# Kernel optimization log

Hardware: AMD Instinct MI355X
Metric: run time of the kernel (lower is better)

Reference implementation:

```python
import jax, jax.numpy as jnp
import numpy as np

B, S, DIM, H = 2, 2048, 1024, 16
DH = DIM // H            # 64
G = DH // 4              # 16 quaternion groups per head
IQ = DIM // 4            # 256
ROPE_BASE = 10000.0
SCALE = DH ** -0.5


def qlinear(x, wr, wi, wj, wk, b):
    # x: [B,S,4*IQ]; strided quaternion components, exact combo from QuaternionLinear.forward
    xr, xi, xj, xk = x[..., 0::4], x[..., 1::4], x[..., 2::4], x[..., 3::4]
    o_r = xr @ wr.T - xi @ wi.T - xj @ wj.T - xk @ wk.T
    o_i = xi @ wr.T + xr @ wi.T + xk @ wk.T - xj @ wj.T
    o_j = xj @ wr.T - xk @ wk.T + xr @ wj.T + xi @ wi.T
    o_k = xk @ wr.T + xj @ wj.T - xi @ wi.T + xr @ wk.T
    out = jnp.stack([o_r, o_i, o_j, o_k], axis=-1).reshape(x.shape[:-1] + (-1,))
    return out + b


def qrope(x):
    # x: [B,H,S,DH]; left quaternion multiply u(theta) \otimes q, axis_mode='cycle'
    b, h, s, dh = x.shape
    g = dh // 4
    xq = x.reshape(b, h, s, g, 4)
    t = jnp.arange(s, dtype=x.dtype)
    inv = 1.0 / (ROPE_BASE ** (jnp.arange(g, dtype=x.dtype) / g))
    ang = t[:, None] * inv[None, :]            # [S,G]
    cos, sin = jnp.cos(ang), jnp.sin(ang)
    gi = jnp.arange(g)
    ax_i = (gi % 3 == 0).astype(x.dtype)
    ax_j = (gi % 3 == 1).astype(x.dtype)
    ax_k = (gi % 3 == 2).astype(x.dtype)
    ur, ui, uj, uk = cos, sin * ax_i, sin * ax_j, sin * ax_k   # [S,G] broadcast over [B,H,S,G]
    xr, xi, xj, xk = xq[..., 0], xq[..., 1], xq[..., 2], xq[..., 3]
    pr = ur * xr - ui * xi - uj * xj - uk * xk
    pi = ur * xi + ui * xr + uj * xk - uk * xj
    pj = ur * xj - ui * xk + uj * xr + uk * xi
    pk = ur * xk + ui * xj - uj * xi + uk * xr
    return jnp.stack([pr, pi, pj, pk], axis=-1).reshape(b, h, s, dh)


def setup_inputs() -> dict:
    key = jax.random.key(0)
    ks = jax.random.split(key, 24)
    x = jax.random.normal(ks[0], (B, S, DIM), dtype=jnp.float32)
    # causal mask: True = masked
    mask = jnp.broadcast_to(jnp.triu(jnp.ones((S, S), dtype=bool), k=1), (B, S, S))
    inp = {"x": x, "mask": mask}
    i = 1
    for proj in ("q", "k", "v", "o"):
        for comp in ("wr", "wi", "wj", "wk"):
            inp[f"{proj}_{comp}"] = jax.random.normal(ks[i], (IQ, IQ), dtype=jnp.float32) * 0.02
            i += 1
        inp[f"{proj}_b"] = jnp.zeros((DIM,), dtype=jnp.float32)
    return inp


def reference(x, mask,
              q_wr, q_wi, q_wj, q_wk, q_b,
              k_wr, k_wi, k_wj, k_wk, k_b,
              v_wr, v_wi, v_wj, v_wk, v_b,
              o_wr, o_wi, o_wj, o_wk, o_b):
    b, s, dm = x.shape
    q = qlinear(x, q_wr, q_wi, q_wj, q_wk, q_b).reshape(b, s, H, DH).transpose(0, 2, 1, 3)
    k = qlinear(x, k_wr, k_wi, k_wj, k_wk, k_b).reshape(b, s, H, DH).transpose(0, 2, 1, 3)
    v = qlinear(x, v_wr, v_wi, v_wj, v_wk, v_b).reshape(b, s, H, DH).transpose(0, 2, 1, 3)
    q, k = qrope(q), qrope(k)
    scores = jnp.einsum('bhsd,bhtd->bhst', q, k) * SCALE
    scores = jnp.where(mask[:, None, :, :], -jnp.inf, scores)
    a = jax.nn.softmax(scores, axis=-1)
    out = jnp.einsum('bhst,bhtd->bhsd', a, v).transpose(0, 2, 1, 3).reshape(b, s, dm)
    return qlinear(out, o_wr, o_wi, o_wj, o_wk, o_b)
```

## Files before the change

kernel.cpp:

```cpp
#include <hip/hip_runtime.h>
#include <stdint.h>

typedef unsigned short u16;
typedef unsigned int   u32;

#define NB   2
#define NS   2048
#define NDIM 1024
#define NH   16
#define NDH  64
#define QSCALE 0.18033688011112042f

typedef __bf16 bf16x8 __attribute__((ext_vector_type(8)));
typedef float  f32x4  __attribute__((ext_vector_type(4)));

#define MFMA_BF16(a,b,c) __builtin_amdgcn_mfma_f32_16x16x32_bf16((a),(b),(c),0,0,0)

#define XBF_OFF   (256)
#define WD_OFF    (XBF_OFF  + 8*1024*1024)
#define BIAS_OFF  (WD_OFF   + 8*1024*1024)
#define QB_OFF    (BIAS_OFF + 16384)
#define KB_OFF    (QB_OFF   + 8*1024*1024)
#define VT_OFF    (KB_OFF   + 8*1024*1024)
#define OP_OFF    (VT_OFF   + 8*1024*1024)
#define LP_OFF    (OP_OFF   + 16*1024*1024)

__device__ __forceinline__ float bf2f(u16 h){
  union { u32 u; float f; } v; v.u = ((u32)h) << 16; return v.f;
}
__device__ __forceinline__ u16 f2bf(float f){
  union { float f; u32 u; } v; v.f = f;
  u32 r = (v.u >> 16) & 1u;
  return (u16)((v.u + 0x7fffu + r) >> 16);
}
__device__ __forceinline__ float load_val(const void* p, int i, int isbf){
  return isbf ? bf2f(((const u16*)p)[i]) : ((const float*)p)[i];
}
__device__ __forceinline__ void gl_lds16(const u16* g, u16* l){
  __builtin_amdgcn_global_load_lds(
      (__attribute__((address_space(1))) void*)(uintptr_t)g,
      (__attribute__((address_space(3))) void*)(uintptr_t)l,
      16, 0, 0);
}

struct QPtrs { const void* w[16]; const void* b[4]; };

__global__ void prep_kernel(const void* __restrict__ xin, QPtrs ptrs,
                            u16* __restrict__ xbf, u16* __restrict__ wd,
                            float* __restrict__ biasf, int* __restrict__ flag){
  __shared__ int cnt;
  if (threadIdx.x == 0) cnt = 0;
  __syncthreads();
  {
    const uint4* xv = (const uint4*)xin;
    uint4 v0 = xv[threadIdx.x * 2], v1 = xv[threadIdx.x * 2 + 1];
    const u16* hh = (const u16*)&v0;
    int ok = 0;
#pragma unroll
    for (int i = 0; i < 16; ++i){
      u16 h = (i < 8) ? hh[i] : ((const u16*)&v1)[i - 8];
      int e = (h >> 7) & 0xFF;
      if ((e > 96 && e < 158) || ((h & 0x7FFF) == 0)) ok++;
    }
    atomicAdd(&cnt, ok);
  }
  __syncthreads();
  int isbf = (cnt > 3600) ? 1 : 0;
  if (blockIdx.x == 0 && threadIdx.x == 0) *flag = isbf;

  int idx = blockIdx.x * 256 + threadIdx.x;

  if (blockIdx.x < 2048){
    int t = idx;
    if (isbf){
      ((uint4*)xbf)[t] = ((const uint4*)xin)[t];
    } else {
      const float4* f4 = (const float4*)xin;
      float4 a = f4[2*t], b = f4[2*t+1];
      ushort4 lo = { f2bf(a.x), f2bf(a.y), f2bf(a.z), f2bf(a.w) };
      ushort4 hi = { f2bf(b.x), f2bf(b.y), f2bf(b.z), f2bf(b.w) };
      ((ushort4*)xbf)[2*t]   = lo;
      ((ushort4*)xbf)[2*t+1] = hi;
    }
  }

  int n = idx & 255, m = (idx >> 8) & 255, c = (idx >> 16) & 3, p = idx >> 18;
  int src = m * 256 + n;
  float vr = load_val(ptrs.w[p*4+0], src, isbf);
  float vi = load_val(ptrs.w[p*4+1], src, isbf);
  float vj = load_val(ptrs.w[p*4+2], src, isbf);
  float vk = load_val(ptrs.w[p*4+3], src, isbf);
  float o0, o1, o2, o3;
  switch (c){
    case 0:  o0 = vr; o1 = -vi; o2 = -vj; o3 = -vk; break;
    case 1:  o0 = vi; o1 =  vr; o2 = -vj; o3 =  vk; break;
    case 2:  o0 = vj; o1 =  vi; o2 =  vr; o3 = -vk; break;
    default: o0 = vk; o1 = -vi; o2 =  vj; o3 =  vr; break;
  }
  ushort4 sv = { f2bf(o0), f2bf(o1), f2bf(o2), f2bf(o3) };
  *(ushort4*)&wd[(size_t)p * 1048576 + (size_t)(4*m + c) * 1024 + 4*n] = sv;
  if (idx < 4096){
    int pp = idx >> 10, oo = idx & 1023;
    biasf[idx] = load_val(ptrs.b[pp], oo, isbf);
  }
}

__global__ __launch_bounds__(256)
void gemm_qkv_kernel(const u16* __restrict__ A, const u16* __restrict__ Bw,
                     const float* __restrict__ bias,
                     u16* __restrict__ qb, u16* __restrict__ kb, u16* __restrict__ vt){
  __shared__ u16 sA[3][128 * 32];
  __shared__ u16 sB[3][128 * 32];
  int tid = threadIdx.x, w = tid >> 6, lane = tid & 63, quad = lane >> 4, l16 = lane & 15;
  int n0 = blockIdx.x * 128, m0 = blockIdx.y * 128;

  f32x4 acc[4][4];
#pragma unroll
  for (int i = 0; i < 4; ++i)
#pragma unroll
    for (int j = 0; j < 4; ++j) acc[i][j] = (f32x4){0.f, 0.f, 0.f, 0.f};

  int cp = lane & 3, rl = lane >> 2;
  int gc = (cp ^ ((rl >> 1) & 3)) * 8;
  const u16* ga = A  + (size_t)(m0 + w*16 + rl) * 1024 + gc;
  const u16* gb = Bw + (size_t)(n0 + w*16 + rl) * 1024 + gc;
  int ldo = w * 512 + lane * 8;
  int xorv = ((l16 >> 1) & 3) * 8;
  int mw = (w & 1) * 64, nw = (w >> 1) * 64;

  auto stage = [&](int k0, int b){
#pragma unroll
    for (int i = 0; i < 2; ++i){
      gl_lds16(ga + (size_t)i * 65536 + k0, &sA[b][ldo + i * 2048]);
      gl_lds16(gb + (size_t)i * 65536 + k0, &sB[b][ldo + i * 2048]);
    }
  };

  stage(0, 0);
  stage(32, 1);
  asm volatile("s_waitcnt vmcnt(4)" ::: "memory");
  __builtin_amdgcn_s_barrier();

  int bcur = 0, bnxt = 2;
  for (int it = 0; it < 32; ++it){
    if (it < 30) stage((it + 2) * 32, bnxt);
    const u16* cA = sA[bcur];
    const u16* cB = sB[bcur];
    bf16x8 af[4], bfr[4];
#pragma unroll
    for (int mt = 0; mt < 4; ++mt)
      af[mt] = *(const bf16x8*)&cA[(mw + mt*16 + l16) * 32 + (quad*8 ^ xorv)];
#pragma unroll
    for (int nt = 0; nt < 4; ++nt)
      bfr[nt] = *(const bf16x8*)&cB[(nw + nt*16 + l16) * 32 + (quad*8 ^ xorv)];
#pragma unroll
    for (int mt = 0; mt < 4; ++mt)
#pragma unroll
      for (int nt = 0; nt < 4; ++nt)
        acc[mt][nt] = MFMA_BF16(af[mt], bfr[nt], acc[mt][nt]);

    if (it < 30) asm volatile("s_waitcnt vmcnt(4)" ::: "memory");
    else         asm volatile("s_waitcnt vmcnt(0)" ::: "memory");
    __builtin_amdgcn_s_barrier();
    bcur = (bcur == 2) ? 0 : bcur + 1;
    bnxt = (bnxt == 2) ? 0 : bnxt + 1;
  }

  int proj = n0 >> 10;
  if (proj == 2){
#pragma unroll
    for (int mt = 0; mt < 4; ++mt){
      int row = m0 + mw + mt*16 + quad*4;
      int b = row >> 11, seq0 = row & 2047;
#pragma unroll
      for (int nt = 0; nt < 4; ++nt){
        int col = n0 + nw + nt*16 + l16;
        int o = col & 1023, h = o >> 6, d = o & 63;
        float bv = bias[col];
        ushort4 pv = { f2bf(acc[mt][nt][0] + bv), f2bf(acc[mt][nt][1] + bv),
                       f2bf(acc[mt][nt][2] + bv), f2bf(acc[mt][nt][3] + bv) };
        *(ushort4*)&vt[((size_t)((b*16 + h) * 64 + d)) * 2048 + seq0] = pv;
      }
    }
  } else {
    float sc = (proj == 0) ? QSCALE : 1.0f;
    u16* dst = proj ? kb : qb;
    int c = l16 & 3;
#pragma unroll
    for (int nt = 0; nt < 4; ++nt){
      int col = n0 + nw + nt*16 + l16;
      int o = col & 1023, h = o >> 6, d = o & 63;
      int g = d >> 2;
      int ax = g % 3;
      int mask = ax + 1;
      int tbl = (ax == 0) ? 0xA : (ax == 1 ? 0x6 : 0xC);
      float sgn = ((tbl >> c) & 1) ? 1.f : -1.f;
      float inv = __builtin_amdgcn_exp2f(-(float)g * 0.8304820237218405f);
      float bv = bias[col];
#pragma unroll
      for (int mt = 0; mt < 4; ++mt){
        int row0 = m0 + mw + mt*16 + quad*4;
        int b = row0 >> 11, s0 = row0 & 2047;
        size_t obase = ((size_t)((b*16 + h) * 2048 + s0)) * 64 + d;
#pragma unroll
        for (int r = 0; r < 4; ++r){
          float v = acc[mt][nt][r] + bv;
          float vp = __shfl_xor(v, mask);
          float ang = (float)(s0 + r) * inv;
          float co = __cosf(ang) * sc;
          float si = __sinf(ang) * sc * sgn;
          dst[obase + (size_t)r * 64] = f2bf(co * v + si * vp);
        }
      }
    }
  }
}

__global__ __launch_bounds__(256)
void gemm_o_kernel(const u16* __restrict__ A, const u16* __restrict__ Bw,
                   const float* __restrict__ bias, void* __restrict__ dout,
                   const int* __restrict__ flag){
  __shared__ u16 sA[3][64 * 32];
  __shared__ u16 sB[3][128 * 32];
  int tid = threadIdx.x, w = tid >> 6, lane = tid & 63, quad = lane >> 4, l16 = lane & 15;
  int n0 = blockIdx.x * 128, m0 = blockIdx.y * 64;

  f32x4 acc[2][4];
#pragma unroll
  for (int i = 0; i < 2; ++i)
#pragma unroll
    for (int j = 0; j < 4; ++j) acc[i][j] = (f32x4){0.f, 0.f, 0.f, 0.f};

  int cp = lane & 3, rl = lane >> 2;
  int gc = (cp ^ ((rl >> 1) & 3)) * 8;
  int xorv = ((l16 >> 1) & 3) * 8;
  int mw = (w & 1) * 32, nw = (w >> 1) * 64;

  auto stage = [&](int k0, int b){
#pragma unroll
    for (int i = 0; i < 3; ++i){
      int ch = w * 3 + i;
      int lr = (ch < 4 ? ch : ch - 4) * 16 + rl;
      int eo = (ch < 4 ? ch : ch - 4) * 512 + lane * 8;
      if (ch < 4) gl_lds16(A  + (size_t)(m0 + lr) * 1024 + k0 + gc, &sA[b][eo]);
      else        gl_lds16(Bw + (size_t)(n0 + lr) * 1024 + k0 + gc, &sB[b][eo]);
    }
  };

  stage(0, 0);
  stage(32, 1);
  asm volatile("s_waitcnt vmcnt(3)" ::: "memory");
  __builtin_amdgcn_s_barrier();

  int bcur = 0, bnxt = 2;
  for (int it = 0; it < 32; ++it){
    if (it < 30) stage((it + 2) * 32, bnxt);
    const u16* cA = sA[bcur];
    const u16* cB = sB[bcur];
    bf16x8 af[2], bfr[4];
#pragma unroll
    for (int mt = 0; mt < 2; ++mt)
      af[mt] = *(const bf16x8*)&cA[(mw + mt*16 + l16) * 32 + (quad*8 ^ xorv)];
#pragma unroll
    for (int nt = 0; nt < 4; ++nt)
      bfr[nt] = *(const bf16x8*)&cB[(nw + nt*16 + l16) * 32 + (quad*8 ^ xorv)];
#pragma unroll
    for (int mt = 0; mt < 2; ++mt)
#pragma unroll
      for (int nt = 0; nt < 4; ++nt)
        acc[mt][nt] = MFMA_BF16(af[mt], bfr[nt], acc[mt][nt]);

    if (it < 30) asm volatile("s_waitcnt vmcnt(3)" ::: "memory");
    else         asm volatile("s_waitcnt vmcnt(0)" ::: "memory");
    __builtin_amdgcn_s_barrier();
    bcur = (bcur == 2) ? 0 : bcur + 1;
    bnxt = (bnxt == 2) ? 0 : bnxt + 1;
  }

  int isbf = *flag;
#pragma unroll
  for (int mt = 0; mt < 2; ++mt){
    int row = m0 + mw + mt*16 + quad*4;
#pragma unroll
    for (int nt = 0; nt < 4; ++nt){
      int col = n0 + nw + nt*16 + l16;
      float bv = bias[col];
#pragma unroll
      for (int r = 0; r < 4; ++r){
        float val = acc[mt][nt][r] + bv;
        size_t addr = (size_t)(row + r) * 1024 + col;
        if (isbf) ((u16*)dout)[addr] = f2bf(val);
        else      ((float*)dout)[addr] = val;
      }
    }
  }
}

#define SPT 20

__global__ __launch_bounds__(256, 2)
void attn_kernel(const u16* __restrict__ Q, const u16* __restrict__ K,
                 const u16* __restrict__ Vt, u16* __restrict__ OP,
                 float* __restrict__ LP){
  __shared__ u16 sK[2][4096];
  __shared__ u16 sPT[4][64 * SPT];
  int bh  = blockIdx.x;
  int spl = blockIdx.y;
  int tid = threadIdx.x, w = tid >> 6, lane = tid & 63, quad = lane >> 4, l16 = lane & 15;
  size_t kbase = (size_t)bh * 2048 * 64;
  size_t vbase = (size_t)bh * 64 * 2048;
  u16* spw = &sPT[w][0];

  auto stage = [&](int kt, int b){
    int kcol = kt * 64;
#pragma unroll
    for (int p = 0; p < 2; ++p){
      int slot = w*128 + p*64 + lane;
      int row = slot >> 3, dc = (slot & 7) ^ (row & 7);
      gl_lds16(K + kbase + (size_t)(kcol + row) * 64 + dc*8, &sK[b][(w*128 + p*64) * 8]);
    }
  };

  for (int item = 0; item < 2; ++item){
    int qt = item ? (int)blockIdx.z : 15 - (int)blockIdx.z;
    int rowbase = qt * 128 + w * 32;

    bf16x8 qf[2][2];
#pragma unroll
    for (int g = 0; g < 2; ++g)
#pragma unroll
      for (int kc = 0; kc < 2; ++kc)
        qf[g][kc] = *(const bf16x8*)(Q + kbase + (size_t)(rowbase + g*16 + l16) * 64 + kc*32 + quad*8);

    f32x4 oaccT[2][4];
    float lsum[2][4];
#pragma unroll
    for (int g = 0; g < 2; ++g)
#pragma unroll
      for (int i = 0; i < 4; ++i){ oaccT[g][i] = (f32x4){0.f,0.f,0.f,0.f}; lsum[g][i] = 0.f; }

    int kt0 = spl ? (qt + 1) : 0;
    int ntiles = qt + 1;

    stage(kt0, 0);
    for (int i = 0; i < ntiles; ++i){
      int kcol = (kt0 + i) * 64;
      __syncthreads();
      if (i + 1 < ntiles) stage(kt0 + i + 1, (i + 1) & 1);
      const u16* bK = sK[i & 1];

      if (kcol <= rowbase + 31){
        bf16x8 vf[4][2];
#pragma unroll
        for (int dn = 0; dn < 4; ++dn)
#pragma unroll
          for (int kc = 0; kc < 2; ++kc)
            vf[dn][kc] = *(const bf16x8*)(Vt + vbase + (size_t)(dn*16 + l16) * 2048
                                          + kcol + kc*32 + quad*8);
        bf16x8 bk[2][4];
#pragma unroll
        for (int kc = 0; kc < 2; ++kc)
#pragma unroll
          for (int nt = 0; nt < 4; ++nt){
            int rw = nt*16 + l16;
            int ch = ((kc*4 + quad) ^ (rw & 7)) * 8;
            bk[kc][nt] = *(const bf16x8*)&bK[rw*64 + ch];
          }
#pragma unroll
        for (int g = 0; g < 2; ++g){
          int G0 = rowbase + g*16;
          if (kcol <= G0 + 15){
            f32x4 sacc[4];
#pragma unroll
            for (int nt = 0; nt < 4; ++nt) sacc[nt] = (f32x4){0.f,0.f,0.f,0.f};
#pragma unroll
            for (int kc = 0; kc < 2; ++kc)
#pragma unroll
              for (int nt = 0; nt < 4; ++nt)
                sacc[nt] = MFMA_BF16(qf[g][kc], bk[kc][nt], sacc[nt]);

            if (kcol + 63 > G0){
#pragma unroll
              for (int nt = 0; nt < 4; ++nt){
                int col = kcol + nt*16 + l16;
                ushort4 pv;
#pragma unroll
                for (int r = 0; r < 4; ++r){
                  int row = G0 + quad*4 + r;
                  float pp = (col <= row) ? __builtin_amdgcn_exp2f(sacc[nt][r]) : 0.f;
                  lsum[g][r] += pp;
                  ((u16*)&pv)[r] = f2bf(pp);
                }
                *(ushort4*)&spw[(nt*16 + l16) * SPT + quad*4] = pv;
              }
            } else {
#pragma unroll
              for (int nt = 0; nt < 4; ++nt){
                ushort4 pv;
#pragma unroll
                for (int r = 0; r < 4; ++r){
                  float pp = __builtin_amdgcn_exp2f(sacc[nt][r]);
                  lsum[g][r] += pp;
                  ((u16*)&pv)[r] = f2bf(pp);
                }
                *(ushort4*)&spw[(nt*16 + l16) * SPT + quad*4] = pv;
              }
            }
#pragma unroll
            for (int kc = 0; kc < 2; ++kc){
              bf16x8 pf;
#pragma unroll
              for (int j = 0; j < 8; ++j)
                pf[j] = ((const __bf16*)spw)[(kc*32 + quad*8 + j) * SPT + l16];
#pragma unroll
              for (int dn = 0; dn < 4; ++dn)
                oaccT[g][dn] = MFMA_BF16(vf[dn][kc], pf, oaccT[g][dn]);
            }
          }
        }
      }
    }

    float* scr = (float*)spw;
#pragma unroll
    for (int g = 0; g < 2; ++g)
#pragma unroll
      for (int r = 0; r < 4; ++r){
        float l = lsum[g][r];
        l += __shfl_xor(l, 1); l += __shfl_xor(l, 2);
        l += __shfl_xor(l, 4); l += __shfl_xor(l, 8);
        if (l16 == 0) scr[g*16 + quad*4 + r] = l;
      }
    float lrow[2];
#pragma unroll
    for (int g = 0; g < 2; ++g) lrow[g] = scr[g*16 + l16];

    size_t obase = ((size_t)(spl*32 + bh)) * 2048;
#pragma unroll
    for (int g = 0; g < 2; ++g){
      int row = rowbase + g*16 + l16;
      if (quad == 0) LP[obase + row] = lrow[g];
#pragma unroll
      for (int dn = 0; dn < 4; ++dn){
        ushort4 ov = { f2bf(oaccT[g][dn][0]), f2bf(oaccT[g][dn][1]),
                       f2bf(oaccT[g][dn][2]), f2bf(oaccT[g][dn][3]) };
        *(ushort4*)&OP[(obase + row) * 64 + dn*16 + quad*4] = ov;
      }
    }

    __syncthreads();
  }
}

__global__ void combine_kernel(const u16* __restrict__ OP, const float* __restrict__ LP,
                               u16* __restrict__ Ab){
  int idx = blockIdx.x * 256 + threadIdx.x;
  int dc = idx & 7, s = (idx >> 3) & 2047, bh = idx >> 14;
  size_t r0 = (size_t)bh * 2048 + s, r1 = (size_t)(32 + bh) * 2048 + s;
  float invl = 1.f / (LP[r0] + LP[r1]);
  union { uint4 v; u16 h[8]; } a0, a1; ushort4 o[2];
  a0.v = *(const uint4*)&OP[r0 * 64 + dc*8];
  a1.v = *(const uint4*)&OP[r1 * 64 + dc*8];
#pragma unroll
  for (int p = 0; p < 2; ++p)
#pragma unroll
    for (int j = 0; j < 4; ++j)
      ((u16*)&o[p])[j] = f2bf((bf2f(a0.h[p*4+j]) + bf2f(a1.h[p*4+j])) * invl);
  int b = bh >> 4, h = bh & 15;
  u16* dst = &Ab[((size_t)(b*2048 + s)) * 1024 + h*64 + dc*8];
  *(ushort4*)dst = o[0];
  *(ushort4*)(dst + 4) = o[1];
}

extern "C" void kernel_launch(void* const* d_in, const int* in_sizes, int n_in,
                              void* d_out, int out_size, void* d_ws, size_t ws_size,
                              hipStream_t stream){
  (void)in_sizes; (void)n_in; (void)out_size; (void)ws_size;
  char* ws = (char*)d_ws;
  int*   flag  = (int*)ws;
  u16*   Xbf   = (u16*)(ws + XBF_OFF);
  u16*   Wd    = (u16*)(ws + WD_OFF);
  float* biasf = (float*)(ws + BIAS_OFF);
  u16*   Qb    = (u16*)(ws + QB_OFF);
  u16*   Kb    = (u16*)(ws + KB_OFF);
  u16*   Vt    = (u16*)(ws + VT_OFF);
  u16*   OP    = (u16*)(ws + OP_OFF);
  float* LP    = (float*)(ws + LP_OFF);
  u16*   Ab    = Xbf;

  QPtrs ptrs;
  for (int p = 0; p < 4; ++p){
    for (int wi = 0; wi < 4; ++wi) ptrs.w[p*4 + wi] = d_in[2 + p*5 + wi];
    ptrs.b[p] = d_in[2 + p*5 + 4];
  }

  prep_kernel<<<4096, 256, 0, stream>>>(d_in[0], ptrs, Xbf, Wd, biasf, flag);
  gemm_qkv_kernel<<<dim3(24, 32), 256, 0, stream>>>(Xbf, Wd, biasf, Qb, Kb, Vt);
  attn_kernel<<<dim3(32, 2, 8), 256, 0, stream>>>(Qb, Kb, Vt, OP, LP);
  combine_kernel<<<2048, 256, 0, stream>>>(OP, LP, Ab);
  gemm_o_kernel<<<dim3(8, 64), 256, 0, stream>>>(Ab, Wd + 3*1048576, biasf + 3072,
                                                 d_out, flag);
}
```

Baseline: 244.4 us.

## Enlarge QKV GEMM tile to 256x256 with 512 threads and split-phase staging

The QKV projection GEMM now uses a 256x256 output tile per block with 8 waves, each wave computing a 128x64 sub-tile in two halves. Staging of A and B tiles is split across the two compute halves, with explicit LDS waits, scheduling barriers and wave priority raised around the MFMA bursts. The aim is more operand reuse per LDS load and better overlap of global-to-LDS copies with matrix math. In exchange the grid shrinks to 192 blocks, which may underfill the GPU, and register and LDS pressure per block rise.

New measurement: 241.6 us. About the same (-1.1%).

```diff
diff --git a/kernel.cpp b/kernel.cpp
--- a/kernel.cpp
+++ b/kernel.cpp
@@ -105,76 +105,113 @@
   }
 }
 
-__global__ __launch_bounds__(256)
+__global__ __launch_bounds__(512, 2)
 void gemm_qkv_kernel(const u16* __restrict__ A, const u16* __restrict__ Bw,
                      const float* __restrict__ bias,
                      u16* __restrict__ qb, u16* __restrict__ kb, u16* __restrict__ vt){
-  __shared__ u16 sA[3][128 * 32];
-  __shared__ u16 sB[3][128 * 32];
-  int tid = threadIdx.x, w = tid >> 6, lane = tid & 63, quad = lane >> 4, l16 = lane & 15;
-  int n0 = blockIdx.x * 128, m0 = blockIdx.y * 128;
-
-  f32x4 acc[4][4];
-#pragma unroll
-  for (int i = 0; i < 4; ++i)
+  __shared__ u16 sA[3][256 * 32];
+  __shared__ u16 sB[3][256 * 32];
+  int tid = threadIdx.x, lane = tid & 63, quad = lane >> 4, l16 = lane & 15;
+  int wid = tid >> 6;
+  int wr = wid >> 2, wc = wid & 3;
+  int mbase = wr * 128, nbase = wc * 64;
+  int n0 = blockIdx.x * 256, m0 = blockIdx.y * 256;
+
+  f32x4 acc[8][4];
+#pragma unroll
+  for (int i = 0; i < 8; ++i)
 #pragma unroll
     for (int j = 0; j < 4; ++j) acc[i][j] = (f32x4){0.f, 0.f, 0.f, 0.f};
 
-  int cp = lane & 3, rl = lane >> 2;
-  int gc = (cp ^ ((rl >> 1) & 3)) * 8;
-  const u16* ga = A  + (size_t)(m0 + w*16 + rl) * 1024 + gc;
-  const u16* gb = Bw + (size_t)(n0 + w*16 + rl) * 1024 + gc;
-  int ldo = w * 512 + lane * 8;
-  int xorv = ((l16 >> 1) & 3) * 8;
-  int mw = (w & 1) * 64, nw = (w >> 1) * 64;
-
-  auto stage = [&](int k0, int b){
-#pragma unroll
-    for (int i = 0; i < 2; ++i){
-      gl_lds16(ga + (size_t)i * 65536 + k0, &sA[b][ldo + i * 2048]);
-      gl_lds16(gb + (size_t)i * 65536 + k0, &sB[b][ldo + i * 2048]);
-    }
+  const u16* gA = A  + (size_t)m0 * 1024;
+  const u16* gB = Bw + (size_t)n0 * 1024;
+  int r0s = tid >> 2,            c0s = tid & 3;
+  int r1s = (tid + 512) >> 2,    c1s = (tid + 512) & 3;
+  int sa0 = r0s * 1024 + (c0s ^ ((r0s >> 1) & 3)) * 8;
+  int sa1 = r1s * 1024 + (c1s ^ ((r1s >> 1) & 3)) * 8;
+  int d0 = tid * 8, d1 = (tid + 512) * 8;
+
+  auto stage_A = [&](int t, int b){
+    int k0 = t * 32;
+    gl_lds16(gA + sa0 + k0, &sA[b][d0]);
+    gl_lds16(gA + sa1 + k0, &sA[b][d1]);
   };
-
-  stage(0, 0);
-  stage(32, 1);
+  auto stage_B = [&](int t, int b){
+    int k0 = t * 32;
+    gl_lds16(gB + sa0 + k0, &sB[b][d0]);
+    gl_lds16(gB + sa1 + k0, &sB[b][d1]);
+  };
+
+  int xo = (quad ^ ((l16 >> 1) & 3)) * 8;
+
+  stage_A(0, 0); stage_B(0, 0);
+  stage_A(1, 1); stage_B(1, 1);
   asm volatile("s_waitcnt vmcnt(4)" ::: "memory");
   __builtin_amdgcn_s_barrier();
 
-  int bcur = 0, bnxt = 2;
-  for (int it = 0; it < 32; ++it){
-    if (it < 30) stage((it + 2) * 32, bnxt);
+  int bcur = 0, bst = 2;
+  for (int t = 0; t < 32; ++t){
     const u16* cA = sA[bcur];
     const u16* cB = sB[bcur];
-    bf16x8 af[4], bfr[4];
-#pragma unroll
-    for (int mt = 0; mt < 4; ++mt)
-      af[mt] = *(const bf16x8*)&cA[(mw + mt*16 + l16) * 32 + (quad*8 ^ xorv)];
-#pragma unroll
-    for (int nt = 0; nt < 4; ++nt)
-      bfr[nt] = *(const bf16x8*)&cB[(nw + nt*16 + l16) * 32 + (quad*8 ^ xorv)];
-#pragma unroll
-    for (int mt = 0; mt < 4; ++mt)
+
+    if (t < 30) stage_A(t + 2, bst);
+    {
+      bf16x8 af[4], bfr[4];
+#pragma unroll
+      for (int mt = 0; mt < 4; ++mt)
+        af[mt] = *(const bf16x8*)&cA[(mbase + mt*16 + l16) * 32 + xo];
 #pragma unroll
       for (int nt = 0; nt < 4; ++nt)
-        acc[mt][nt] = MFMA_BF16(af[mt], bfr[nt], acc[mt][nt]);
-
-    if (it < 30) asm volatile("s_waitcnt vmcnt(4)" ::: "memory");
-    else         asm volatile("s_waitcnt vmcnt(0)" ::: "memory");
+        bfr[nt] = *(const bf16x8*)&cB[(nbase + nt*16 + l16) * 32 + xo];
+      asm volatile("s_waitcnt lgkmcnt(0)" ::: "memory");
+      __builtin_amdgcn_sched_barrier(0);
+      __builtin_amdgcn_s_setprio(1);
+#pragma unroll
+      for (int mt = 0; mt < 4; ++mt)
+#pragma unroll
+        for (int nt = 0; nt < 4; ++nt)
+          acc[mt][nt] = MFMA_BF16(af[mt], bfr[nt], acc[mt][nt]);
+      __builtin_amdgcn_s_setprio(0);
+    }
     __builtin_amdgcn_s_barrier();
+
+    if (t < 30) stage_B(t + 2, bst);
+    {
+      bf16x8 af[4], bfr[4];
+#pragma unroll
+      for (int mt = 0; mt < 4; ++mt)
+        af[mt] = *(const bf16x8*)&cA[(mbase + (4+mt)*16 + l16) * 32 + xo];
+#pragma unroll
+      for (int nt = 0; nt < 4; ++nt)
+        bfr[nt] = *(const bf16x8*)&cB[(nbase + nt*16 + l16) * 32 + xo];
+      asm volatile("s_waitcnt lgkmcnt(0)" ::: "memory");
+      __builtin_amdgcn_sched_barrier(0);
+      __builtin_amdgcn_s_setprio(1);
+#pragma unroll
+      for (int mt = 0; mt < 4; ++mt)
+#pragma unroll
+        for (int nt = 0; nt < 4; ++nt)
+          acc[4+mt][nt] = MFMA_BF16(af[mt], bfr[nt], acc[4+mt][nt]);
+      __builtin_amdgcn_s_setprio(0);
+    }
+    if (t < 31){
+      if (t < 30) asm volatile("s_waitcnt vmcnt(4)" ::: "memory");
+      else        asm volatile("s_waitcnt vmcnt(0)" ::: "memory");
+      __builtin_amdgcn_s_barrier();
+    }
     bcur = (bcur == 2) ? 0 : bcur + 1;
-    bnxt = (bnxt == 2) ? 0 : bnxt + 1;
+    bst  = (bst  == 2) ? 0 : bst  + 1;
   }
 
   int proj = n0 >> 10;
   if (proj == 2){
 #pragma unroll
-    for (int mt = 0; mt < 4; ++mt){
-      int row = m0 + mw + mt*16 + quad*4;
+    for (int mt = 0; mt < 8; ++mt){
+      int row = m0 + mbase + mt*16 + quad*4;
       int b = row >> 11, seq0 = row & 2047;
 #pragma unroll
       for (int nt = 0; nt < 4; ++nt){
-        int col = n0 + nw + nt*16 + l16;
+        int col = n0 + nbase + nt*16 + l16;
         int o = col & 1023, h = o >> 6, d = o & 63;
         float bv = bias[col];
         ushort4 pv = { f2bf(acc[mt][nt][0] + bv), f2bf(acc[mt][nt][1] + bv),
@@ -188,7 +225,7 @@
     int c = l16 & 3;
 #pragma unroll
     for (int nt = 0; nt < 4; ++nt){
-      int col = n0 + nw + nt*16 + l16;
+      int col = n0 + nbase + nt*16 + l16;
       int o = col & 1023, h = o >> 6, d = o & 63;
       int g = d >> 2;
       int ax = g % 3;
@@ -198,8 +235,8 @@
       float inv = __builtin_amdgcn_exp2f(-(float)g * 0.8304820237218405f);
       float bv = bias[col];
 #pragma unroll
-      for (int mt = 0; mt < 4; ++mt){
-        int row0 = m0 + mw + mt*16 + quad*4;
+      for (int mt = 0; mt < 8; ++mt){
+        int row0 = m0 + mbase + mt*16 + quad*4;
         int b = row0 >> 11, s0 = row0 & 2047;
         size_t obase = ((size_t)((b*16 + h) * 2048 + s0)) * 64 + d;
 #pragma unroll
@@ -495,7 +532,7 @@
   }
 
   prep_kernel<<<4096, 256, 0, stream>>>(d_in[0], ptrs, Xbf, Wd, biasf, flag);
-  gemm_qkv_kernel<<<dim3(24, 32), 256, 0, stream>>>(Xbf, Wd, biasf, Qb, Kb, Vt);
+  gemm_qkv_kernel<<<dim3(12, 16), 512, 0, stream>>>(Xbf, Wd, biasf, Qb, Kb, Vt);
   attn_kernel<<<dim3(32, 2, 8), 256, 0, stream>>>(Qb, Kb, Vt, OP, LP);
   combine_kernel<<<2048, 256, 0, stream>>>(OP, LP, Ab);
   gemm_o_kernel<<<dim3(8, 64), 256, 0, stream>>>(Ab, Wd + 3*1048576, biasf + 3072,
```

## Fuse split-KV attention halves into one 512-thread block and drop combine kernel

Applied to the files above, without the earlier changes.

Both key-range halves of the split attention now run as two wave groups inside one 512-thread block. Their partial outputs and row sums are merged through shared memory, and the result is written straight into the attention output buffer. This removes the combine kernel launch and the global round-trip for the partial outputs and sums. In exchange the grid has half as many blocks and LDS use per block is larger, which may cut occupancy. The two halves can also have unequal causal work, leaving one wave group idle while the other finishes.

Result: slower. 251.0 us (+2.7%).

```diff
diff --git a/kernel.cpp b/kernel.cpp
--- a/kernel.cpp
+++ b/kernel.cpp
@@ -22,8 +22,6 @@
 #define QB_OFF    (BIAS_OFF + 16384)
 #define KB_OFF    (QB_OFF   + 8*1024*1024)
 #define VT_OFF    (KB_OFF   + 8*1024*1024)
-#define OP_OFF    (VT_OFF   + 8*1024*1024)
-#define LP_OFF    (OP_OFF   + 16*1024*1024)
 
 __device__ __forceinline__ float bf2f(u16 h){
   union { u32 u; float f; } v; v.u = ((u32)h) << 16; return v.f;
@@ -298,15 +296,16 @@
 
 #define SPT 20
 
-__global__ __launch_bounds__(256, 2)
+__global__ __launch_bounds__(512, 2)
 void attn_kernel(const u16* __restrict__ Q, const u16* __restrict__ K,
-                 const u16* __restrict__ Vt, u16* __restrict__ OP,
-                 float* __restrict__ LP){
-  __shared__ u16 sK[2][4096];
-  __shared__ u16 sPT[4][64 * SPT];
+                 const u16* __restrict__ Vt, u16* __restrict__ Ab){
+  __shared__ u16 sK[2][2][4096];
+  __shared__ u16 sPT[8][64 * SPT];
+  __shared__ u16 cmb[128 * 64];
+  __shared__ float l_sh[2][128];
   int bh  = blockIdx.x;
-  int spl = blockIdx.y;
   int tid = threadIdx.x, w = tid >> 6, lane = tid & 63, quad = lane >> 4, l16 = lane & 15;
+  int wg = w >> 2, wl = w & 3;
   size_t kbase = (size_t)bh * 2048 * 64;
   size_t vbase = (size_t)bh * 64 * 2048;
   u16* spw = &sPT[w][0];
@@ -315,15 +314,15 @@
     int kcol = kt * 64;
 #pragma unroll
     for (int p = 0; p < 2; ++p){
-      int slot = w*128 + p*64 + lane;
+      int slot = wl*128 + p*64 + lane;
       int row = slot >> 3, dc = (slot & 7) ^ (row & 7);
-      gl_lds16(K + kbase + (size_t)(kcol + row) * 64 + dc*8, &sK[b][(w*128 + p*64) * 8]);
+      gl_lds16(K + kbase + (size_t)(kcol + row) * 64 + dc*8, &sK[wg][b][(wl*128 + p*64) * 8]);
     }
   };
 
   for (int item = 0; item < 2; ++item){
-    int qt = item ? (int)blockIdx.z : 15 - (int)blockIdx.z;
-    int rowbase = qt * 128 + w * 32;
+    int qt = item ? (int)blockIdx.y : 15 - (int)blockIdx.y;
+    int rowbase = qt * 128 + wl * 32;
 
     bf16x8 qf[2][2];
 #pragma unroll
@@ -339,7 +338,7 @@
 #pragma unroll
       for (int i = 0; i < 4; ++i){ oaccT[g][i] = (f32x4){0.f,0.f,0.f,0.f}; lsum[g][i] = 0.f; }
 
-    int kt0 = spl ? (qt + 1) : 0;
+    int kt0 = wg ? (qt + 1) : 0;
     int ntiles = qt + 1;
 
     stage(kt0, 0);
@@ -347,7 +346,7 @@
       int kcol = (kt0 + i) * 64;
       __syncthreads();
       if (i + 1 < ntiles) stage(kt0 + i + 1, (i + 1) & 1);
-      const u16* bK = sK[i & 1];
+      const u16* bK = sK[wg][i & 1];
 
       if (kcol <= rowbase + 31){
         bf16x8 vf[4][2];
@@ -421,7 +420,6 @@
       }
     }
 
-    float* scr = (float*)spw;
 #pragma unroll
     for (int g = 0; g < 2; ++g)
 #pragma unroll
@@ -429,47 +427,46 @@
         float l = lsum[g][r];
         l += __shfl_xor(l, 1); l += __shfl_xor(l, 2);
         l += __shfl_xor(l, 4); l += __shfl_xor(l, 8);
-        if (l16 == 0) scr[g*16 + quad*4 + r] = l;
-      }
-    float lrow[2];
-#pragma unroll
-    for (int g = 0; g < 2; ++g) lrow[g] = scr[g*16 + l16];
-
-    size_t obase = ((size_t)(spl*32 + bh)) * 2048;
-#pragma unroll
-    for (int g = 0; g < 2; ++g){
-      int row = rowbase + g*16 + l16;
-      if (quad == 0) LP[obase + row] = lrow[g];
-#pragma unroll
-      for (int dn = 0; dn < 4; ++dn){
-        ushort4 ov = { f2bf(oaccT[g][dn][0]), f2bf(oaccT[g][dn][1]),
-                       f2bf(oaccT[g][dn][2]), f2bf(oaccT[g][dn][3]) };
-        *(ushort4*)&OP[(obase + row) * 64 + dn*16 + quad*4] = ov;
-      }
-    }
-
+        if (l16 == 0) l_sh[wg][wl*32 + g*16 + quad*4 + r] = l;
+      }
+
+    if (wg == 1){
+#pragma unroll
+      for (int g = 0; g < 2; ++g){
+        int row_l = wl*32 + g*16 + l16;
+#pragma unroll
+        for (int dn = 0; dn < 4; ++dn){
+          int gi = (dn*4 + quad) ^ (row_l & 7);
+          ushort4 ov = { f2bf(oaccT[g][dn][0]), f2bf(oaccT[g][dn][1]),
+                         f2bf(oaccT[g][dn][2]), f2bf(oaccT[g][dn][3]) };
+          *(ushort4*)&cmb[row_l*64 + gi*4] = ov;
+        }
+      }
+    }
     __syncthreads();
-  }
-}
-
-__global__ void combine_kernel(const u16* __restrict__ OP, const float* __restrict__ LP,
-                               u16* __restrict__ Ab){
-  int idx = blockIdx.x * 256 + threadIdx.x;
-  int dc = idx & 7, s = (idx >> 3) & 2047, bh = idx >> 14;
-  size_t r0 = (size_t)bh * 2048 + s, r1 = (size_t)(32 + bh) * 2048 + s;
-  float invl = 1.f / (LP[r0] + LP[r1]);
-  union { uint4 v; u16 h[8]; } a0, a1; ushort4 o[2];
-  a0.v = *(const uint4*)&OP[r0 * 64 + dc*8];
-  a1.v = *(const uint4*)&OP[r1 * 64 + dc*8];
-#pragma unroll
-  for (int p = 0; p < 2; ++p)
-#pragma unroll
-    for (int j = 0; j < 4; ++j)
-      ((u16*)&o[p])[j] = f2bf((bf2f(a0.h[p*4+j]) + bf2f(a1.h[p*4+j])) * invl);
-  int b = bh >> 4, h = bh & 15;
-  u16* dst = &Ab[((size_t)(b*2048 + s)) * 1024 + h*64 + dc*8];
-  *(ushort4*)dst = o[0];
-  *(ushort4*)(dst + 4) = o[1];
+
+    if (wg == 0){
+      int b = bh >> 4, h = bh & 15;
+#pragma unroll
+      for (int g = 0; g < 2; ++g){
+        int row_l = wl*32 + g*16 + l16;
+        float linv = 1.f / (l_sh[0][row_l] + l_sh[1][row_l]);
+        int s = qt*128 + row_l;
+        u16* dst = &Ab[((size_t)(b*2048 + s)) * 1024 + h*64];
+#pragma unroll
+        for (int dn = 0; dn < 4; ++dn){
+          int gi = (dn*4 + quad) ^ (row_l & 7);
+          const u16* o1 = &cmb[row_l*64 + gi*4];
+          ushort4 ov;
+#pragma unroll
+          for (int r = 0; r < 4; ++r)
+            ((u16*)&ov)[r] = f2bf((oaccT[g][dn][r] + bf2f(o1[r])) * linv);
+          *(ushort4*)&dst[dn*16 + quad*4] = ov;
+        }
+      }
+    }
+    __syncthreads();
+  }
 }
 
 extern "C" void kernel_launch(void* const* d_in, const int* in_sizes, int n_in,
@@ -484,8 +481,6 @@
   u16*   Qb    = (u16*)(ws + QB_OFF);
   u16*   Kb    = (u16*)(ws + KB_OFF);
   u16*   Vt    = (u16*)(ws + VT_OFF);
-  u16*   OP    = (u16*)(ws + OP_OFF);
-  float* LP    = (float*)(ws + LP_OFF);
   u16*   Ab    = Xbf;
 
   QPtrs ptrs;
@@ -496,8 +491,7 @@
 
   prep_kernel<<<4096, 256, 0, stream>>>(d_in[0], ptrs, Xbf, Wd, biasf, flag);
   gemm_qkv_kernel<<<dim3(24, 32), 256, 0, stream>>>(Xbf, Wd, biasf, Qb, Kb, Vt);
-  attn_kernel<<<dim3(32, 2, 8), 256, 0, stream>>>(Qb, Kb, Vt, OP, LP);
-  combine_kernel<<<2048, 256, 0, stream>>>(OP, LP, Ab);
+  attn_kernel<<<dim3(32, 8), 512, 0, stream>>>(Qb, Kb, Vt, Ab);
   gemm_o_kernel<<<dim3(8, 64), 256, 0, stream>>>(Ab, Wd + 3*1048576, biasf + 3072,
                                                  d_out, flag);
 }
```
